# Performance work log

Hardware: AMD Instinct MI355X
Metric: run time of the kernel (lower is better)

Reference implementation:

```python
import jax, jax.numpy as jnp
import numpy as np
from jax import lax

N, T, V, E, H, D, B = 16384, 16, 10000, 256, 256, 512, 128


def setup_inputs() -> dict:
    key = jax.random.key(0)
    ks = jax.random.split(key, 12)
    tok = jax.random.randint(ks[0], (N, T), 1, V)
    lens = jax.random.randint(ks[1], (N,), 4, T + 1)
    tok = jnp.where(jnp.arange(T)[None, :] < lens[:, None], tok, 0)  # pad_id = 0
    ast_path_len = jnp.full((B,), N // B, dtype=jnp.int32)  # 128 paths per sample
    u = lambda k, s: jax.random.uniform(k, s, jnp.float32, -0.1, 0.1)
    emb = u(ks[2], (V, E)).at[0].set(0.0)  # padding_idx=0 row zeroed
    return {
        "ast_path": tok,
        "ast_path_len": ast_path_len,
        "emb": emb,
        "W_ih_f": u(ks[3], (4 * H, E)), "W_hh_f": u(ks[4], (4 * H, H)), "b_f": u(ks[5], (4 * H,)),
        "W_ih_b": u(ks[6], (4 * H, E)), "W_hh_b": u(ks[7], (4 * H, H)), "b_b": u(ks[8], (4 * H,)),
        "W_lin": u(ks[9], (D, 2 * H)), "b_lin": jnp.zeros((D,), jnp.float32),
    }


def _lstm_final_h(x_tm, lens, W_ih, W_hh, b, reverse):
    # x_tm: [T, N, E]; returns final hidden state [N, H] honoring per-seq length
    n = x_tm.shape[1]
    h0 = jnp.zeros((n, H), x_tm.dtype)

    def step(carry, xt):
        h, c = carry
        x, t = xt
        gates = x @ W_ih.T + h @ W_hh.T + b  # [N, 4H]
        i, f, g, o = jnp.split(gates, 4, axis=-1)
        c_new = jax.nn.sigmoid(f) * c + jax.nn.sigmoid(i) * jnp.tanh(g)
        h_new = jax.nn.sigmoid(o) * jnp.tanh(c_new)
        m = (t < lens)[:, None]  # packed-sequence semantics: frozen past length
        return (jnp.where(m, h_new, h), jnp.where(m, c_new, c)), None

    (h, _), _ = lax.scan(step, (h0, h0), (x_tm, jnp.arange(x_tm.shape[0])), reverse=reverse)
    return h


def reference(ast_path, ast_path_len, emb, W_ih_f, W_hh_f, b_f, W_ih_b, W_hh_b, b_b, W_lin, b_lin):
    lens = (ast_path != 0).sum(axis=-1)  # pad_id = 0
    x = emb[ast_path]                     # [N, T, E]; dropout is identity at eval
    x_tm = jnp.swapaxes(x, 0, 1)          # [T, N, E]
    h_fwd = _lstm_final_h(x_tm, lens, W_ih_f, W_hh_f, b_f, reverse=False)
    h_bwd = _lstm_final_h(x_tm, lens, W_ih_b, W_hh_b, b_b, reverse=True)
    h_n = jnp.concatenate([h_fwd, h_bwd], axis=1)        # [N, 2H]
    repr_ = h_n @ W_lin.T + b_lin                         # [N, D]
    # segment-mean pooling over path groups (replaces the Python loop)
    n_paths = repr_.shape[0]
    seg_ids = jnp.repeat(jnp.arange(ast_path_len.shape[0]), ast_path_len,
                         total_repeat_length=n_paths)
    sums = jax.ops.segment_sum(repr_, seg_ids, num_segments=ast_path_len.shape[0])
    pooled = sums / ast_path_len[:, None].astype(repr_.dtype)  # [B, D]
    norm = jnp.sqrt(jnp.sum(pooled * pooled, axis=-1, keepdims=True))
    return pooled / jnp.maximum(norm, 1e-5)
```

## Files before the change

### kernel.cpp

```cpp
#include <hip/hip_runtime.h>
#include <stdint.h>

#define N_SEQ 16384
#define T_LEN 16
#define E_DIM 256
#define H_DIM 256
#define K_DIM 512
#define B_SAMP 128
#define V_SIZE 10000

typedef __bf16 bf16x8 __attribute__((ext_vector_type(8)));
typedef float  f32x4  __attribute__((ext_vector_type(4)));
typedef unsigned short ush;

__device__ __forceinline__ ush f2bf(float x) {
  unsigned int u = __float_as_uint(x);
  u = (u + 0x7fffu + ((u >> 16) & 1u)) >> 16;
  return (ush)u;
}
__device__ __forceinline__ float bf2f(ush v) {
  return __uint_as_float(((unsigned int)v) << 16);
}
__device__ __forceinline__ float sigmoidf_(float x) {
  return 1.0f / (1.0f + __expf(-x));
}
__device__ __forceinline__ float tanhf_(float x) {
  float e = __expf(2.0f * x);
  return 1.0f - 2.0f / (e + 1.0f);
}
__device__ __forceinline__ void glds16(const void* g, const void* l) {
  __builtin_amdgcn_global_load_lds(
      (const __attribute__((address_space(1))) unsigned int*)g,
      (__attribute__((address_space(3))) unsigned int*)l, 16, 0, 0);
}


__global__ __launch_bounds__(256) void k_lens(const int* __restrict__ tok, int* __restrict__ lens,
                                              int* __restrict__ hist) {
  __shared__ int lh[17];
  if (threadIdx.x < 17) lh[threadIdx.x] = 0;
  __syncthreads();
  int n = blockIdx.x * 256 + threadIdx.x;
  const int* r = tok + n * T_LEN;
  int c = 0;
#pragma unroll
  for (int t = 0; t < T_LEN; ++t) c += (r[t] != 0);
  lens[n] = c;
  atomicAdd(&lh[c], 1);
  __syncthreads();
  if (threadIdx.x < 17 && lh[threadIdx.x]) atomicAdd(&hist[threadIdx.x], lh[threadIdx.x]);
}

__global__ void k_offsets(const int* __restrict__ hist, int* __restrict__ cursor,
                          int* __restrict__ cnts_f, int* __restrict__ cnts_b) {
  if (threadIdx.x == 0) {
    int off = 0;
    for (int l = 16; l >= 0; --l) { cursor[l] = off; off += hist[l]; }
    for (int t = 0; t < 16; ++t) {
      int cf = 0, cb = 0;
      for (int l = t; l <= 16; ++l) cf += hist[l];
      for (int l = t + 1; l <= 16; ++l) cb += hist[l];
      cnts_f[t] = cf;
      cnts_b[t] = cb;
    }
  }
}

__global__ __launch_bounds__(256) void k_scatter(const int* __restrict__ lens, int* __restrict__ cursor,
                                                 int* __restrict__ perm, int* __restrict__ pinv,
                                                 int* __restrict__ plens) {
  int n = blockIdx.x * 256 + threadIdx.x;
  int l = lens[n];
  int pos = atomicAdd(&cursor[l], 1);
  perm[pos] = n;
  pinv[n] = pos;
  plens[pos] = l;
}

__global__ __launch_bounds__(256) void k_tokperm(const int* __restrict__ tok, const int* __restrict__ perm,
                                                 int* __restrict__ tokperm) {
  int id = blockIdx.x * 256 + threadIdx.x;
  int t = id >> 14;
  int pos = id & (N_SEQ - 1);
  tokperm[id] = tok[perm[pos] * T_LEN + t];
}

__global__ __launch_bounds__(256) void k_embcvt(const float* __restrict__ emb, ush* __restrict__ out) {
  int i = blockIdx.x * 256 + threadIdx.x;
  out[i] = f2bf(emb[i]);
}

__global__ __launch_bounds__(256) void k_wprep(const float* __restrict__ Wih_f, const float* __restrict__ Whh_f,
                                               const float* __restrict__ Wih_b, const float* __restrict__ Whh_b,
                                               ush* __restrict__ wpt_f, ush* __restrict__ wpt_b) {
  int id = blockIdx.x * 256 + threadIdx.x;
  int dir = id >> 19;
  int rem = id & ((1 << 19) - 1);
  int p = rem >> 9;
  int k = rem & 511;
  int nb = p >> 7, wcl = (p >> 6) & 1, q = (p >> 4) & 3, jj = p & 15;
  int r = q * 256 + nb * 32 + wcl * 16 + jj;
  const float* Wih = dir ? Wih_b : Wih_f;
  const float* Whh = dir ? Whh_b : Whh_f;
  float v = (k < 256) ? Wih[r * 256 + k] : Whh[r * 256 + (k - 256)];
  ush* o = dir ? wpt_b : wpt_f;
  o[p * 512 + k] = f2bf(v);
}


__global__ __launch_bounds__(256, 2)
void k_step(const ush* __restrict__ embbf, const int* __restrict__ tokperm,
            const int* __restrict__ plens,
            const int* __restrict__ cnts_f, const int* __restrict__ cnts_b,
            const ush* __restrict__ wpt_f, const ush* __restrict__ wpt_b,
            const float* __restrict__ bias_f, const float* __restrict__ bias_b,
            const ush* __restrict__ hr_f, ush* __restrict__ hw_f,
            const ush* __restrict__ hr_b, ush* __restrict__ hw_b,
            float* __restrict__ cT_f, float* __restrict__ cT_b,
            int s) {
  const int b = blockIdx.x;
  const int dir = b & 1;
  const int nblk = ((b >> 1) & 3) * 2 + ((b >> 3) & 1);
  const int rt = b >> 4;
  const int t = dir ? (15 - s) : s;
  const int cnt = dir ? cnts_b[t] : cnts_f[t];
  const int m0 = rt * 128;
  if (m0 >= cnt) return;

  const ush* wpt = dir ? wpt_b : wpt_f;
  const float* bias = dir ? bias_b : bias_f;
  const ush* hr = dir ? hr_b : hr_f;
  ush* hw = dir ? hw_b : hw_f;
  float* cT = dir ? cT_b : cT_f;

  __shared__ __align__(128) unsigned char lds[2][32768];

  const int tid = threadIdx.x;
  const int lane = tid & 63;
  const int w = tid >> 6;
  const int wr = w >> 1, wc = w & 1;
  const int l8 = lane >> 3, l7 = lane & 7;
  const int frow = lane & 15, fkq = lane >> 4;

  unsigned aoffE[4], aoffH[4], boff[4];
#pragma unroll
  for (int i = 0; i < 4; ++i) {
    const int arow = 32 * w + 8 * i + l8;
    const int ach = l7 ^ (arow & 7);
    aoffE[i] = (unsigned)tokperm[t * N_SEQ + m0 + arow] * (E_DIM * 2) + ach * 16;
    aoffH[i] = (unsigned)(m0 + arow) * (H_DIM * 2) + ach * 16;
    boff[i]  = (unsigned)(nblk * 128 + arow) * (K_DIM * 2) + ach * 16;
  }
  const char* embc = (const char*)embbf;
  const char* hrc  = (const char*)hr;
  const char* wptc = (const char*)wpt;

  f32x4 acc[4][4] = {};

  auto stage = [&](int kt, int buf) {
    if (kt < 4) {
      const int ak = kt * 128;
#pragma unroll
      for (int i = 0; i < 4; ++i)
        glds16(embc + aoffE[i] + ak, &lds[buf][(32 * w + 8 * i) * 128]);
    } else {
      const int ak = (kt - 4) * 128;
#pragma unroll
      for (int i = 0; i < 4; ++i)
        glds16(hrc + aoffH[i] + ak, &lds[buf][(32 * w + 8 * i) * 128]);
    }
#pragma unroll
    for (int i = 0; i < 4; ++i)
      glds16(wptc + boff[i] + kt * 128, &lds[buf][16384 + (32 * w + 8 * i) * 128]);
  };
  auto compute = [&](int buf) {
#pragma unroll
    for (int ksub = 0; ksub < 2; ++ksub) {
      const int slot = ksub * 4 + fkq;
      bf16x8 av[4], bv[4];
#pragma unroll
      for (int fr = 0; fr < 4; ++fr) {
        const int row = wr * 64 + fr * 16 + frow;
        av[fr] = *(const bf16x8*)&lds[buf][row * 128 + ((slot ^ (row & 7)) * 16)];
      }
#pragma unroll
      for (int fc = 0; fc < 4; ++fc) {
        const int prow = wc * 64 + fc * 16 + frow;
        bv[fc] = *(const bf16x8*)&lds[buf][16384 + prow * 128 + ((slot ^ (prow & 7)) * 16)];
      }
      __builtin_amdgcn_s_setprio(1);
#pragma unroll
      for (int fr = 0; fr < 4; ++fr)
#pragma unroll
        for (int fc = 0; fc < 4; ++fc)
          acc[fr][fc] = __builtin_amdgcn_mfma_f32_16x16x32_bf16(av[fr], bv[fc], acc[fr][fc], 0, 0, 0);
      __builtin_amdgcn_s_setprio(0);
    }
  };

  stage(0, 0);
  stage(1, 1);
#pragma unroll
  for (int kt = 0; kt < 8; ++kt) {
    if (kt <= 6) asm volatile("s_waitcnt vmcnt(8)" ::: "memory");
    else         asm volatile("s_waitcnt vmcnt(0)" ::: "memory");
    __builtin_amdgcn_s_barrier();
    __builtin_amdgcn_sched_barrier(0);
    compute(kt & 1);
    if (kt <= 5) {
      __builtin_amdgcn_s_barrier();
      __builtin_amdgcn_sched_barrier(0);
      stage(kt + 2, kt & 1);
    }
  }

  const int j = nblk * 32 + wc * 16 + frow;
  const float b0 = bias[j], b1 = bias[256 + j], b2 = bias[512 + j], b3 = bias[768 + j];
#pragma unroll
  for (int fr = 0; fr < 4; ++fr) {
    const int n0 = m0 + wr * 64 + fr * 16 + fkq * 4;
    const int4 l4 = *(const int4*)&plens[n0];
    f32x4 cv = *(const f32x4*)&cT[(size_t)j * N_SEQ + n0];
    const f32x4 gi = acc[fr][0], gf = acc[fr][1], gg = acc[fr][2], go = acc[fr][3];
#pragma unroll
    for (int r = 0; r < 4; ++r) {
      const int lnv = (r == 0) ? l4.x : (r == 1) ? l4.y : (r == 2) ? l4.z : l4.w;
      const size_t hidx = (size_t)(n0 + r) * H_DIM + j;
      if (t < lnv) {
        const float iv = sigmoidf_(gi[r] + b0);
        const float fv = sigmoidf_(gf[r] + b1);
        const float gv = tanhf_(gg[r] + b2);
        const float ov = sigmoidf_(go[r] + b3);
        const bool first = dir ? (t == lnv - 1) : (t == 0);
        const float cn = fv * (first ? 0.0f : cv[r]) + iv * gv;
        cv[r] = cn;
        hw[hidx] = f2bf(ov * tanhf_(cn));
      } else if (!dir) {
        hw[hidx] = hr[hidx];
      }
    }
    *(f32x4*)&cT[(size_t)j * N_SEQ + n0] = cv;
  }
}


__global__ __launch_bounds__(256) void k_pool(const ush* __restrict__ hf,
                                              const ush* __restrict__ hb,
                                              const int* __restrict__ pinv,
                                              const int* __restrict__ plen,
                                              float* __restrict__ pooled) {
  const int b = blockIdx.x, tid = threadIdx.x;
  int start = 0;
  for (int i = 0; i < b; ++i) start += plen[i];
  const int cnt = plen[b];
  float s0 = 0.f, s1 = 0.f;
  for (int r = 0; r < cnt; ++r) {
    const size_t pr = (size_t)pinv[start + r];
    s0 += bf2f(hf[pr * H_DIM + tid]);
    s1 += bf2f(hb[pr * H_DIM + tid]);
  }
  float inv = 1.0f / (float)cnt;
  pooled[b * 512 + tid] = s0 * inv;
  pooled[b * 512 + H_DIM + tid] = s1 * inv;
}


__global__ __launch_bounds__(256) void k_final(const float* __restrict__ pooled,
                                               const float* __restrict__ W,
                                               const float* __restrict__ bl,
                                               float* __restrict__ out) {
  const int b = blockIdx.x, tid = threadIdx.x;
  __shared__ float pv[512];
  __shared__ float pre[512];
  __shared__ float red[4];
  pv[tid] = pooled[b * 512 + tid];
  pv[tid + 256] = pooled[b * 512 + 256 + tid];
  __syncthreads();
#pragma unroll
  for (int half = 0; half < 2; ++half) {
    const int dd = tid + half * 256;
    const f32x4* wr = (const f32x4*)(W + (size_t)dd * 512);
    const f32x4* pvv = (const f32x4*)pv;
    float s = bl[dd];
#pragma unroll 4
    for (int k4 = 0; k4 < 128; ++k4) {
      f32x4 wv = wr[k4], xv = pvv[k4];
      s += wv[0] * xv[0] + wv[1] * xv[1] + wv[2] * xv[2] + wv[3] * xv[3];
    }
    pre[dd] = s;
  }
  __syncthreads();
  float ss = pre[tid] * pre[tid] + pre[tid + 256] * pre[tid + 256];
#pragma unroll
  for (int off = 32; off > 0; off >>= 1) ss += __shfl_down(ss, off, 64);
  if ((tid & 63) == 0) red[tid >> 6] = ss;
  __syncthreads();
  float tot = red[0] + red[1] + red[2] + red[3];
  float scale = 1.0f / fmaxf(sqrtf(tot), 1e-5f);
  out[b * 512 + tid] = pre[tid] * scale;
  out[b * 512 + 256 + tid] = pre[tid + 256] * scale;
}


extern "C" void kernel_launch(void* const* d_in, const int* in_sizes, int n_in,
                              void* d_out, int out_size, void* d_ws, size_t ws_size,
                              hipStream_t stream) {
  const int* tok    = (const int*)d_in[0];
  const int* plen   = (const int*)d_in[1];
  const float* emb  = (const float*)d_in[2];
  const float* Wih_f = (const float*)d_in[3];
  const float* Whh_f = (const float*)d_in[4];
  const float* b_f   = (const float*)d_in[5];
  const float* Wih_b = (const float*)d_in[6];
  const float* Whh_b = (const float*)d_in[7];
  const float* b_b   = (const float*)d_in[8];
  const float* Wlin  = (const float*)d_in[9];
  const float* blin  = (const float*)d_in[10];
  float* out = (float*)d_out;

  char* ws = (char*)d_ws;
  size_t off = 0;
  auto alloc = [&](size_t bytes) {
    void* p = ws + off;
    off = (off + bytes + 255) & ~(size_t)255;
    return p;
  };
  ush* embbf   = (ush*)alloc((size_t)V_SIZE * E_DIM * 2);
  ush* wptf    = (ush*)alloc((size_t)1024 * K_DIM * 2);
  ush* wptb    = (ush*)alloc((size_t)1024 * K_DIM * 2);
  int* lens    = (int*)alloc((size_t)N_SEQ * 4);
  int* perm    = (int*)alloc((size_t)N_SEQ * 4);
  int* pinv    = (int*)alloc((size_t)N_SEQ * 4);
  int* plens   = (int*)alloc((size_t)N_SEQ * 4);
  int* tokperm = (int*)alloc((size_t)T_LEN * N_SEQ * 4);
  int* hist    = (int*)alloc(17 * 4);
  int* cursor  = (int*)alloc(17 * 4);
  int* cntsf   = (int*)alloc(16 * 4);
  int* cntsb   = (int*)alloc(16 * 4);
  ush* h0f     = (ush*)alloc((size_t)N_SEQ * H_DIM * 2);
  ush* h1f     = (ush*)alloc((size_t)N_SEQ * H_DIM * 2);
  ush* h0b     = (ush*)alloc((size_t)N_SEQ * H_DIM * 2);
  ush* h1b     = (ush*)alloc((size_t)N_SEQ * H_DIM * 2);
  float* cTf   = (float*)alloc((size_t)H_DIM * N_SEQ * 4);
  float* cTb   = (float*)alloc((size_t)H_DIM * N_SEQ * 4);
  float* pooled = (float*)alloc((size_t)B_SAMP * 512 * 4);

  hipMemsetAsync(hist, 0, 17 * 4, stream);
  hipMemsetAsync(h0f, 0, (size_t)N_SEQ * H_DIM * 2, stream);
  hipMemsetAsync(h1f, 0, (size_t)N_SEQ * H_DIM * 2, stream);
  hipMemsetAsync(h0b, 0, (size_t)N_SEQ * H_DIM * 2, stream);
  hipMemsetAsync(h1b, 0, (size_t)N_SEQ * H_DIM * 2, stream);

  k_lens<<<N_SEQ / 256, 256, 0, stream>>>(tok, lens, hist);
  k_offsets<<<1, 64, 0, stream>>>(hist, cursor, cntsf, cntsb);
  k_scatter<<<N_SEQ / 256, 256, 0, stream>>>(lens, cursor, perm, pinv, plens);
  k_tokperm<<<(T_LEN * N_SEQ) / 256, 256, 0, stream>>>(tok, perm, tokperm);
  k_embcvt<<<(V_SIZE * E_DIM) / 256, 256, 0, stream>>>(emb, embbf);
  k_wprep<<<(2 * 1024 * K_DIM) / 256, 256, 0, stream>>>(Wih_f, Whh_f, Wih_b, Whh_b, wptf, wptb);

  for (int s = 0; s < T_LEN; ++s) {
    const ush* hrf = (s & 1) ? h1f : h0f;
    ush* hwf       = (s & 1) ? h0f : h1f;
    const ush* hrb = (s & 1) ? h1b : h0b;
    ush* hwb       = (s & 1) ? h0b : h1b;
    k_step<<<2048, 256, 0, stream>>>(embbf, tokperm, plens, cntsf, cntsb, wptf, wptb,
                                     b_f, b_b, hrf, hwf, hrb, hwb, cTf, cTb, s);
  }
  k_pool<<<B_SAMP, 256, 0, stream>>>(h0f, h0b, pinv, plen, pooled);
  k_final<<<B_SAMP, 256, 0, stream>>>(pooled, Wlin, blin, out);
}
```

Baseline: 979.5 us.

## Make LSTM step kernel persistent with LDS-resident weight panels and 256-row tiles

```diff
diff --git a/kernel.cpp b/kernel.cpp
--- a/kernel.cpp
+++ b/kernel.cpp
@@ -108,7 +108,7 @@
 }
 
 
-__global__ __launch_bounds__(256, 2)
+__global__ __launch_bounds__(512, 2)
 void k_step(const ush* __restrict__ embbf, const int* __restrict__ tokperm,
             const int* __restrict__ plens,
             const int* __restrict__ cnts_f, const int* __restrict__ cnts_b,
@@ -118,128 +118,134 @@
             const ush* __restrict__ hr_b, ush* __restrict__ hw_b,
             float* __restrict__ cT_f, float* __restrict__ cT_b,
             int s) {
-  const int b = blockIdx.x;
-  const int dir = b & 1;
-  const int nblk = ((b >> 1) & 3) * 2 + ((b >> 3) & 1);
-  const int rt = b >> 4;
-  const int t = dir ? (15 - s) : s;
-  const int cnt = dir ? cnts_b[t] : cnts_f[t];
-  const int m0 = rt * 128;
-  if (m0 >= cnt) return;
-
-  const ush* wpt = dir ? wpt_b : wpt_f;
-  const float* bias = dir ? bias_b : bias_f;
-  const ush* hr = dir ? hr_b : hr_f;
-  ush* hw = dir ? hw_b : hw_f;
-  float* cT = dir ? cT_b : cT_f;
-
-  __shared__ __align__(128) unsigned char lds[2][32768];
+  const int tf = s, tb = 15 - s;
+  const int tilesf = (cnts_f[tf] + 255) >> 8;
+  const int tilesb = (cnts_b[tb] + 255) >> 8;
+  const unsigned totf = (unsigned)tilesf * 8u;
+  const unsigned T = totf + (unsigned)tilesb * 8u;
+  const unsigned b = blockIdx.x;
+  const unsigned g0 = (b * T) >> 8;
+  const unsigned g1 = ((b + 1) * T) >> 8;
+  if (g0 >= g1) return;
+
+  __shared__ __align__(128) unsigned char ldsB[131072];
+  __shared__ __align__(128) unsigned char ldsA[2][16384];
 
   const int tid = threadIdx.x;
   const int lane = tid & 63;
   const int w = tid >> 6;
   const int wr = w >> 1, wc = w & 1;
-  const int l8 = lane >> 3, l7 = lane & 7;
   const int frow = lane & 15, fkq = lane >> 4;
-
-  unsigned aoffE[4], aoffH[4], boff[4];
-#pragma unroll
-  for (int i = 0; i < 4; ++i) {
-    const int arow = 32 * w + 8 * i + l8;
-    const int ach = l7 ^ (arow & 7);
-    aoffE[i] = (unsigned)tokperm[t * N_SEQ + m0 + arow] * (E_DIM * 2) + ach * 16;
-    aoffH[i] = (unsigned)(m0 + arow) * (H_DIM * 2) + ach * 16;
-    boff[i]  = (unsigned)(nblk * 128 + arow) * (K_DIM * 2) + ach * 16;
-  }
-  const char* embc = (const char*)embbf;
-  const char* hrc  = (const char*)hr;
-  const char* wptc = (const char*)wpt;
-
-  f32x4 acc[4][4] = {};
-
-  auto stage = [&](int kt, int buf) {
-    if (kt < 4) {
-      const int ak = kt * 128;
-#pragma unroll
-      for (int i = 0; i < 4; ++i)
-        glds16(embc + aoffE[i] + ak, &lds[buf][(32 * w + 8 * i) * 128]);
-    } else {
-      const int ak = (kt - 4) * 128;
-#pragma unroll
-      for (int i = 0; i < 4; ++i)
-        glds16(hrc + aoffH[i] + ak, &lds[buf][(32 * w + 8 * i) * 128]);
-    }
-#pragma unroll
-    for (int i = 0; i < 4; ++i)
-      glds16(wptc + boff[i] + kt * 128, &lds[buf][16384 + (32 * w + 8 * i) * 128]);
-  };
-  auto compute = [&](int buf) {
-#pragma unroll
-    for (int ksub = 0; ksub < 2; ++ksub) {
-      const int slot = ksub * 4 + fkq;
+  const int rr = lane >> 2;
+  const int kk = (lane & 3) * 8;
+
+  int curkey = -1;
+
+  for (unsigned g = g0; g < g1; ++g) {
+    int dir, nblk; unsigned rt;
+    if (g < totf) { dir = 0; nblk = (int)(g / (unsigned)tilesf); rt = g - (unsigned)nblk * tilesf; }
+    else { unsigned gg = g - totf; dir = 1; nblk = (int)(gg / (unsigned)tilesb); rt = gg - (unsigned)nblk * tilesb; }
+    const int t = dir ? tb : tf;
+    const int m0 = (int)rt << 8;
+    const ush* wpt = dir ? wpt_b : wpt_f;
+    const float* bias = dir ? bias_b : bias_f;
+    const ush* hr = dir ? hr_b : hr_f;
+    ush* hw = dir ? hw_b : hw_f;
+    float* cT = dir ? cT_b : cT_f;
+
+    __syncthreads();
+
+    const int key = dir * 8 + nblk;
+    if (key != curkey) {
+      curkey = key;
+      const char* wsrc = (const char*)wpt + (size_t)nblk * 128 * 1024;
+#pragma unroll
+      for (int i = 0; i < 16; ++i) {
+        const int prow = i * 8 + w;
+        glds16(wsrc + (size_t)prow * 1024 + ((lane ^ (prow & 7)) * 16), &ldsB[prow * 1024]);
+      }
+    }
+
+    const int r0 = w * 32 + rr, r1 = r0 + 16;
+    const int n0g = m0 + r0, n1g = m0 + r1;
+    const ush* xsrc0 = embbf + (size_t)tokperm[t * N_SEQ + n0g] * 256 + kk;
+    const ush* xsrc1 = embbf + (size_t)tokperm[t * N_SEQ + n1g] * 256 + kk;
+    const ush* hsrc0 = hr + (size_t)n0g * 256 + kk;
+    const ush* hsrc1 = hr + (size_t)n1g * 256 + kk;
+
+    auto stageA = [&](int kt, int buf) {
+      const int ko = (kt & 7) * 32;
+      const ush* s0 = (kt < 8) ? (xsrc0 + ko) : (hsrc0 + ko);
+      const ush* s1 = (kt < 8) ? (xsrc1 + ko) : (hsrc1 + ko);
+      glds16(s0, &ldsA[buf][(w * 32) * 64]);
+      glds16(s1, &ldsA[buf][(w * 32 + 16) * 64]);
+    };
+
+    f32x4 acc[4][4] = {};
+
+    auto compute = [&](int kt, int buf) {
       bf16x8 av[4], bv[4];
 #pragma unroll
-      for (int fr = 0; fr < 4; ++fr) {
-        const int row = wr * 64 + fr * 16 + frow;
-        av[fr] = *(const bf16x8*)&lds[buf][row * 128 + ((slot ^ (row & 7)) * 16)];
-      }
-#pragma unroll
-      for (int fc = 0; fc < 4; ++fc) {
-        const int prow = wc * 64 + fc * 16 + frow;
-        bv[fc] = *(const bf16x8*)&lds[buf][16384 + prow * 128 + ((slot ^ (prow & 7)) * 16)];
+      for (int fr = 0; fr < 4; ++fr)
+        av[fr] = *(const bf16x8*)&ldsA[buf][(wr * 64 + fr * 16 + frow) * 64 + fkq * 16];
+#pragma unroll
+      for (int q = 0; q < 4; ++q) {
+        const int prow = wc * 64 + q * 16 + frow;
+        const int slot = (kt * 4 + fkq) ^ (prow & 7);
+        bv[q] = *(const bf16x8*)&ldsB[prow * 1024 + slot * 16];
       }
       __builtin_amdgcn_s_setprio(1);
 #pragma unroll
       for (int fr = 0; fr < 4; ++fr)
 #pragma unroll
-        for (int fc = 0; fc < 4; ++fc)
-          acc[fr][fc] = __builtin_amdgcn_mfma_f32_16x16x32_bf16(av[fr], bv[fc], acc[fr][fc], 0, 0, 0);
+        for (int q = 0; q < 4; ++q)
+          acc[fr][q] = __builtin_amdgcn_mfma_f32_16x16x32_bf16(av[fr], bv[q], acc[fr][q], 0, 0, 0);
       __builtin_amdgcn_s_setprio(0);
-    }
-  };
-
-  stage(0, 0);
-  stage(1, 1);
-#pragma unroll
-  for (int kt = 0; kt < 8; ++kt) {
-    if (kt <= 6) asm volatile("s_waitcnt vmcnt(8)" ::: "memory");
-    else         asm volatile("s_waitcnt vmcnt(0)" ::: "memory");
-    __builtin_amdgcn_s_barrier();
-    __builtin_amdgcn_sched_barrier(0);
-    compute(kt & 1);
-    if (kt <= 5) {
+    };
+
+    stageA(0, 0);
+    stageA(1, 1);
+#pragma unroll
+    for (int kt = 0; kt < 16; ++kt) {
+      if (kt < 15) asm volatile("s_waitcnt vmcnt(2)" ::: "memory");
+      else         asm volatile("s_waitcnt vmcnt(0)" ::: "memory");
       __builtin_amdgcn_s_barrier();
       __builtin_amdgcn_sched_barrier(0);
-      stage(kt + 2, kt & 1);
-    }
-  }
-
-  const int j = nblk * 32 + wc * 16 + frow;
-  const float b0 = bias[j], b1 = bias[256 + j], b2 = bias[512 + j], b3 = bias[768 + j];
-#pragma unroll
-  for (int fr = 0; fr < 4; ++fr) {
-    const int n0 = m0 + wr * 64 + fr * 16 + fkq * 4;
-    const int4 l4 = *(const int4*)&plens[n0];
-    f32x4 cv = *(const f32x4*)&cT[(size_t)j * N_SEQ + n0];
-    const f32x4 gi = acc[fr][0], gf = acc[fr][1], gg = acc[fr][2], go = acc[fr][3];
-#pragma unroll
-    for (int r = 0; r < 4; ++r) {
-      const int lnv = (r == 0) ? l4.x : (r == 1) ? l4.y : (r == 2) ? l4.z : l4.w;
-      const size_t hidx = (size_t)(n0 + r) * H_DIM + j;
-      if (t < lnv) {
-        const float iv = sigmoidf_(gi[r] + b0);
-        const float fv = sigmoidf_(gf[r] + b1);
-        const float gv = tanhf_(gg[r] + b2);
-        const float ov = sigmoidf_(go[r] + b3);
-        const bool first = dir ? (t == lnv - 1) : (t == 0);
-        const float cn = fv * (first ? 0.0f : cv[r]) + iv * gv;
-        cv[r] = cn;
-        hw[hidx] = f2bf(ov * tanhf_(cn));
-      } else if (!dir) {
-        hw[hidx] = hr[hidx];
+      compute(kt, kt & 1);
+      if (kt < 14) {
+        __builtin_amdgcn_s_barrier();
+        __builtin_amdgcn_sched_barrier(0);
+        stageA(kt + 2, kt & 1);
       }
     }
-    *(f32x4*)&cT[(size_t)j * N_SEQ + n0] = cv;
+
+    const int j = nblk * 32 + wc * 16 + frow;
+    const float b0 = bias[j], b1 = bias[256 + j], b2 = bias[512 + j], b3 = bias[768 + j];
+#pragma unroll
+    for (int fr = 0; fr < 4; ++fr) {
+      const int n0 = m0 + wr * 64 + fr * 16 + fkq * 4;
+      const int4 l4 = *(const int4*)&plens[n0];
+      f32x4 cv = *(const f32x4*)&cT[(size_t)j * N_SEQ + n0];
+      const f32x4 gi = acc[fr][0], gf = acc[fr][1], gg = acc[fr][2], go = acc[fr][3];
+#pragma unroll
+      for (int r = 0; r < 4; ++r) {
+        const int lnv = (r == 0) ? l4.x : (r == 1) ? l4.y : (r == 2) ? l4.z : l4.w;
+        const size_t hidx = (size_t)(n0 + r) * H_DIM + j;
+        if (t < lnv) {
+          const float iv = sigmoidf_(gi[r] + b0);
+          const float fv = sigmoidf_(gf[r] + b1);
+          const float gv = tanhf_(gg[r] + b2);
+          const float ov = sigmoidf_(go[r] + b3);
+          const bool first = dir ? (t == lnv - 1) : (t == 0);
+          const float cn = fv * (first ? 0.0f : cv[r]) + iv * gv;
+          cv[r] = cn;
+          hw[hidx] = f2bf(ov * tanhf_(cn));
+        } else if (!dir) {
+          hw[hidx] = hr[hidx];
+        }
+      }
+      *(f32x4*)&cT[(size_t)j * N_SEQ + n0] = cv;
+    }
   }
 }
 
@@ -363,8 +369,8 @@
     ush* hwf       = (s & 1) ? h0f : h1f;
     const ush* hrb = (s & 1) ? h1b : h0b;
     ush* hwb       = (s & 1) ? h0b : h1b;
-    k_step<<<2048, 256, 0, stream>>>(embbf, tokperm, plens, cntsf, cntsb, wptf, wptb,
-                                     b_f, b_b, hrf, hwf, hrb, hwb, cTf, cTb, s);
+    k_step<<<256, 512, 0, stream>>>(embbf, tokperm, plens, cntsf, cntsb, wptf, wptb,
+                                    b_f, b_b, hrf, hwf, hrb, hwb, cTf, cTb, s);
   }
   k_pool<<<B_SAMP, 256, 0, stream>>>(h0f, h0b, pinv, plen, pooled);
   k_final<<<B_SAMP, 256, 0, stream>>>(pooled, Wlin, blin, out);
```

Measured after the change: 1.122 ms. +14.5%, slower.
